# Optimization experiments

Hardware: AMD Instinct MI355X
Metric: run time of the kernel (lower is better)

Reference implementation:

```python
import jax, jax.numpy as jnp
import numpy as np

B, H, S, D = 4, 16, 2048, 64

def setup_inputs() -> dict:
    key = jax.random.key(0)
    kq, kk, kv = jax.random.split(key, 3)
    return {
        "query": jax.random.normal(kq, (B, H, S, D), dtype=jnp.float32),
        "key": jax.random.normal(kk, (B, H, S, D), dtype=jnp.float32),
        "value": jax.random.normal(kv, (B, H, S, D), dtype=jnp.float32),
        "dropout_p": 0,
    }

def reference(query, key, value, dropout_p):
    # qk: [B,H,S,S] materialized as in the original (unfused SDPA)
    scale = query.shape[-1] ** -0.5
    qk = jnp.einsum("bhqd,bhkd->bhqk", query, key) * scale
    attn = jax.nn.softmax(qk, axis=-1)
    # dropout_p == 0 -> identity (keeps reference deterministic)
    out = jnp.einsum("bhqk,bhkd->bhqd", attn, value)
    return out
```

## Files before the change

kernel.cpp:

```cpp
#include <hip/hip_runtime.h>
#include <hip/hip_bf16.h>

#define B_   4
#define H_   16
#define SEQ  2048
#define DH   64
#define BM   128
#define BN   128
#define NBH  (B_ * H_)
#define NELEM (NBH * SEQ * DH)

typedef __bf16 bf16x8 __attribute__((ext_vector_type(8)));
typedef float  f32x4  __attribute__((ext_vector_type(4)));
typedef unsigned short u16x8 __attribute__((ext_vector_type(8)));
typedef unsigned short u16x4 __attribute__((ext_vector_type(4)));

__device__ __forceinline__ unsigned short f2bu(float x) {
    __hip_bfloat16 h = __float2bfloat16(x);
    return __builtin_bit_cast(unsigned short, h);
}

__device__ __forceinline__ void ld_lds16(const unsigned short* g, unsigned short* l) {
    __builtin_amdgcn_global_load_lds(
        (const __attribute__((address_space(1))) unsigned int*)(g),
        (__attribute__((address_space(3))) unsigned int*)(l), 16, 0, 0);
}

__global__ __launch_bounds__(256)
void cvt_k_kernel(const float* __restrict__ K, unsigned short* __restrict__ Kb) {
    const int i = (blockIdx.x * 256 + threadIdx.x) * 8;
    const float4 a = *reinterpret_cast<const float4*>(K + i);
    const float4 b = *reinterpret_cast<const float4*>(K + i + 4);
    u16x8 o;
    o[0] = f2bu(a.x); o[1] = f2bu(a.y); o[2] = f2bu(a.z); o[3] = f2bu(a.w);
    o[4] = f2bu(b.x); o[5] = f2bu(b.y); o[6] = f2bu(b.z); o[7] = f2bu(b.w);
    *reinterpret_cast<u16x8*>(Kb + i) = o;
}

__global__ __launch_bounds__(256)
void tr_v_kernel(const float* __restrict__ V, unsigned short* __restrict__ Vt) {
    __shared__ unsigned short tile[64 * 72];
    const int bh = blockIdx.y;
    const int s0 = blockIdx.x * 64;
    const float* Vb = V + (size_t)bh * SEQ * DH + (size_t)s0 * DH;
    unsigned short* Vo = Vt + (size_t)bh * DH * SEQ;
    const int t = threadIdx.x;
    {
        const int sl = t >> 2, d0 = (t & 3) * 16;
        for (int c = 0; c < 4; ++c) {
            const float4 v = *reinterpret_cast<const float4*>(Vb + sl * DH + d0 + c * 4);
            u16x4 u; u[0] = f2bu(v.x); u[1] = f2bu(v.y); u[2] = f2bu(v.z); u[3] = f2bu(v.w);
            *reinterpret_cast<u16x4*>(&tile[sl * 72 + d0 + c * 4]) = u;
        }
    }
    __syncthreads();
    {
        const int d = t >> 2, sc = (t & 3) * 16;
        for (int j = 0; j < 4; ++j) {
            u16x4 u;
            u[0] = tile[(sc + 4 * j + 0) * 72 + d];
            u[1] = tile[(sc + 4 * j + 1) * 72 + d];
            u[2] = tile[(sc + 4 * j + 2) * 72 + d];
            u[3] = tile[(sc + 4 * j + 3) * 72 + d];
            *reinterpret_cast<u16x4*>(Vo + (size_t)d * SEQ + s0 + sc + 4 * j) = u;
        }
    }
}

__global__ __launch_bounds__(256, 2)
void fa_fwd(const float* __restrict__ Qg, const unsigned short* __restrict__ Kb,
            const unsigned short* __restrict__ Vtb, float* __restrict__ Og)
{
    __shared__ __attribute__((aligned(16))) unsigned short smem[32768];
    unsigned short* Klds = smem;
    unsigned short* Vlds = smem + 8192;
    unsigned short* Plds = smem + 16384;

    const int tid  = threadIdx.x;
    const int lane = tid & 63;
    const int wave = tid >> 6;
    const int l15  = lane & 15;
    const int quad = lane >> 4;

    const int qtile = blockIdx.x;
    const int bh    = blockIdx.y;

    const float*          Qb  = Qg  + (size_t)bh * SEQ * DH;
    const unsigned short* Kbh = Kb  + (size_t)bh * SEQ * DH;
    const unsigned short* Vbh = Vtb + (size_t)bh * DH * SEQ;
    float*                Ob  = Og  + (size_t)bh * SEQ * DH;

    const int qrow0 = qtile * BM + wave * 32;

    bf16x8 Qf[2][2];
    for (int rt = 0; rt < 2; ++rt) {
        const float* qsrc = Qb + (size_t)(qrow0 + rt * 16 + l15) * DH + quad * 8;
        for (int kt = 0; kt < 2; ++kt) {
            const float4 a = *reinterpret_cast<const float4*>(qsrc + kt * 32);
            const float4 b = *reinterpret_cast<const float4*>(qsrc + kt * 32 + 4);
            union { bf16x8 v; unsigned short u[8]; } tmp;
            tmp.u[0] = f2bu(a.x); tmp.u[1] = f2bu(a.y); tmp.u[2] = f2bu(a.z); tmp.u[3] = f2bu(a.w);
            tmp.u[4] = f2bu(b.x); tmp.u[5] = f2bu(b.y); tmp.u[6] = f2bu(b.z); tmp.u[7] = f2bu(b.w);
            Qf[rt][kt] = tmp.v;
        }
    }

    f32x4 Oacc[2][4];
    float lsum[2][4];
    for (int rt = 0; rt < 2; ++rt)
        for (int r = 0; r < 4; ++r) lsum[rt][r] = 0.f;
    for (int rt = 0; rt < 2; ++rt)
        for (int dt = 0; dt < 4; ++dt) {
            f32x4 z = {0.f, 0.f, 0.f, 0.f};
            Oacc[rt][dt] = z;
        }

    const float CS   = 0.125f * 1.4426950408889634f;
    const float MFIX = 12.0f;

    for (int it = 0; it < SEQ / BN; ++it) {
        __syncthreads();

        for (int i = 0; i < 4; ++i) {
            const int slot = i * 256 + tid;
            const int s = slot >> 3;
            const int g = (slot & 7) ^ (s & 7);
            ld_lds16(Kbh + (size_t)(it * BN + s) * DH + g * 8,
                     Klds + (size_t)(i * 256 + wave * 64) * 8);
        }
        for (int i = 0; i < 4; ++i) {
            const int slot = i * 256 + tid;
            const int d = slot >> 4;
            const int g = (slot & 15) ^ (d & 15);
            ld_lds16(Vbh + (size_t)d * SEQ + it * BN + g * 8,
                     Vlds + (size_t)(i * 256 + wave * 64) * 8);
        }
        __syncthreads();

        f32x4 Sacc[2][8];
        for (int rt = 0; rt < 2; ++rt)
            for (int nt = 0; nt < 8; ++nt) {
                f32x4 z = {0.f, 0.f, 0.f, 0.f};
                Sacc[rt][nt] = z;
            }
        for (int nt = 0; nt < 8; ++nt) {
            const int s  = nt * 16 + l15;
            const int sx = s & 7;
            const bf16x8 kf0 = *reinterpret_cast<const bf16x8*>(&Klds[s * 64 + ((quad    ) ^ sx) * 8]);
            const bf16x8 kf1 = *reinterpret_cast<const bf16x8*>(&Klds[s * 64 + ((quad + 4) ^ sx) * 8]);
            for (int rt = 0; rt < 2; ++rt) {
                Sacc[rt][nt] = __builtin_amdgcn_mfma_f32_16x16x32_bf16(Qf[rt][0], kf0, Sacc[rt][nt], 0, 0, 0);
                Sacc[rt][nt] = __builtin_amdgcn_mfma_f32_16x16x32_bf16(Qf[rt][1], kf1, Sacc[rt][nt], 0, 0, 0);
            }
        }

        for (int rt = 0; rt < 2; ++rt) {
            for (int r = 0; r < 4; ++r) {
                const int m  = wave * 32 + rt * 16 + quad * 4 + r;
                const int mx = m & 15;
                unsigned short* pb = &Plds[m << 7];
                float lacc = 0.f;
                for (int nt = 0; nt < 8; ++nt) {
                    const float p = __builtin_amdgcn_exp2f(fmaf(Sacc[rt][nt][r], CS, -MFIX));
                    lacc += p;
                    const int gg = nt * 2 + (l15 >> 3);
                    pb[((gg ^ mx) << 3) + (l15 & 7)] = f2bu(p);
                }
                lsum[rt][r] += lacc;
            }
        }

        for (int ks = 0; ks < 4; ++ks) {
            bf16x8 af[2];
            for (int rt = 0; rt < 2; ++rt) {
                const int m = wave * 32 + rt * 16 + l15;
                af[rt] = *reinterpret_cast<const bf16x8*>(
                    &Plds[(m << 7) + (((ks * 4 + quad) ^ l15) << 3)]);
            }
            for (int dt = 0; dt < 4; ++dt) {
                const int d = dt * 16 + l15;
                const bf16x8 bfr = *reinterpret_cast<const bf16x8*>(
                    &Vlds[(d << 7) + (((ks * 4 + quad) ^ l15) << 3)]);
                for (int rt = 0; rt < 2; ++rt)
                    Oacc[rt][dt] = __builtin_amdgcn_mfma_f32_16x16x32_bf16(af[rt], bfr, Oacc[rt][dt], 0, 0, 0);
            }
        }
    }

    for (int rt = 0; rt < 2; ++rt) {
        for (int r = 0; r < 4; ++r) {
            float tot = lsum[rt][r];
            tot += __shfl_xor(tot, 1, 64);
            tot += __shfl_xor(tot, 2, 64);
            tot += __shfl_xor(tot, 4, 64);
            tot += __shfl_xor(tot, 8, 64);
            const float inv = 1.0f / tot;
            const int row = qrow0 + rt * 16 + quad * 4 + r;
            float* orow = Ob + (size_t)row * DH + l15;
            for (int dt = 0; dt < 4; ++dt)
                orow[dt * 16] = Oacc[rt][dt][r] * inv;
        }
    }
}

extern "C" void kernel_launch(void* const* d_in, const int* in_sizes, int n_in,
                              void* d_out, int out_size, void* d_ws, size_t ws_size,
                              hipStream_t stream) {
    const float* Q = (const float*)d_in[0];
    const float* K = (const float*)d_in[1];
    const float* V = (const float*)d_in[2];
    float* O = (float*)d_out;

    unsigned short* Kb = (unsigned short*)d_ws;
    unsigned short* Vt = Kb + (size_t)NELEM;

    cvt_k_kernel<<<NELEM / (256 * 8), 256, 0, stream>>>(K, Kb);
    tr_v_kernel<<<dim3(SEQ / 64, NBH), 256, 0, stream>>>(V, Vt);
    fa_fwd<<<dim3(SEQ / BM, NBH), dim3(256), 0, stream>>>(Q, Kb, Vt, O);
}
```

Before: 245.5 us.

## Shrink P LDS buffer per wave, vectorize P stores, fuse K/V prep kernels

The K tile rows are loaded in a permuted order so each lane's eight softmax probabilities become contiguous keys and can be written to LDS as a single 16-byte store. The PV product is moved inside the per-row-tile loop, which halves the P staging buffer so total LDS drops and launch bounds can target three blocks per CU. The K conversion and V transpose preprocessing are fused into one launch. The trade-off is that the V fragments are now reloaded once per row tile, and register pressure rises at the higher occupancy target.

```diff
diff --git a/kernel.cpp b/kernel.cpp
--- a/kernel.cpp
+++ b/kernel.cpp
@@ -27,24 +27,26 @@
 }
 
 __global__ __launch_bounds__(256)
-void cvt_k_kernel(const float* __restrict__ K, unsigned short* __restrict__ Kb) {
-    const int i = (blockIdx.x * 256 + threadIdx.x) * 8;
-    const float4 a = *reinterpret_cast<const float4*>(K + i);
-    const float4 b = *reinterpret_cast<const float4*>(K + i + 4);
-    u16x8 o;
-    o[0] = f2bu(a.x); o[1] = f2bu(a.y); o[2] = f2bu(a.z); o[3] = f2bu(a.w);
-    o[4] = f2bu(b.x); o[5] = f2bu(b.y); o[6] = f2bu(b.z); o[7] = f2bu(b.w);
-    *reinterpret_cast<u16x8*>(Kb + i) = o;
-}
-
-__global__ __launch_bounds__(256)
-void tr_v_kernel(const float* __restrict__ V, unsigned short* __restrict__ Vt) {
+void prep_kv(const float* __restrict__ K, const float* __restrict__ V,
+             unsigned short* __restrict__ Kb, unsigned short* __restrict__ Vt) {
     __shared__ unsigned short tile[64 * 72];
     const int bh = blockIdx.y;
     const int s0 = blockIdx.x * 64;
+    const int t  = threadIdx.x;
+
+    {
+        const float* Ki = K + (size_t)bh * SEQ * DH + (size_t)s0 * DH;
+        unsigned short* Ko = Kb + (size_t)bh * SEQ * DH + (size_t)s0 * DH;
+        for (int j = 0; j < 4; ++j) {
+            const int e = (j * 256 + t) * 4;
+            const float4 v = *reinterpret_cast<const float4*>(Ki + e);
+            u16x4 u; u[0] = f2bu(v.x); u[1] = f2bu(v.y); u[2] = f2bu(v.z); u[3] = f2bu(v.w);
+            *reinterpret_cast<u16x4*>(Ko + e) = u;
+        }
+    }
+
     const float* Vb = V + (size_t)bh * SEQ * DH + (size_t)s0 * DH;
     unsigned short* Vo = Vt + (size_t)bh * DH * SEQ;
-    const int t = threadIdx.x;
     {
         const int sl = t >> 2, d0 = (t & 3) * 16;
         for (int c = 0; c < 4; ++c) {
@@ -67,11 +69,11 @@
     }
 }
 
-__global__ __launch_bounds__(256, 2)
+__global__ __launch_bounds__(256, 3)
 void fa_fwd(const float* __restrict__ Qg, const unsigned short* __restrict__ Kb,
             const unsigned short* __restrict__ Vtb, float* __restrict__ Og)
 {
-    __shared__ __attribute__((aligned(16))) unsigned short smem[32768];
+    __shared__ __attribute__((aligned(16))) unsigned short smem[24576];
     unsigned short* Klds = smem;
     unsigned short* Vlds = smem + 8192;
     unsigned short* Plds = smem + 16384;
@@ -122,16 +124,18 @@
         __syncthreads();
 
         for (int i = 0; i < 4; ++i) {
-            const int slot = i * 256 + tid;
-            const int s = slot >> 3;
-            const int g = (slot & 7) ^ (s & 7);
-            ld_lds16(Kbh + (size_t)(it * BN + s) * DH + g * 8,
+            const int beta = i * 256 + tid;
+            const int s    = beta >> 3;
+            const int b    = beta & 7;
+            const int gnat = b ^ (s & 7);
+            const int grow = (s & 15) * 8 + (s >> 4);
+            ld_lds16(Kbh + (size_t)(it * BN + grow) * DH + gnat * 8,
                      Klds + (size_t)(i * 256 + wave * 64) * 8);
         }
         for (int i = 0; i < 4; ++i) {
-            const int slot = i * 256 + tid;
-            const int d = slot >> 4;
-            const int g = (slot & 15) ^ (d & 15);
+            const int beta = i * 256 + tid;
+            const int d    = beta >> 4;
+            const int g    = (beta & 15) ^ (d & 15);
             ld_lds16(Vbh + (size_t)d * SEQ + it * BN + g * 8,
                      Vlds + (size_t)(i * 256 + wave * 64) * 8);
         }
@@ -156,33 +160,27 @@
 
         for (int rt = 0; rt < 2; ++rt) {
             for (int r = 0; r < 4; ++r) {
-                const int m  = wave * 32 + rt * 16 + quad * 4 + r;
-                const int mx = m & 15;
-                unsigned short* pb = &Plds[m << 7];
+                const int rho = quad * 4 + r;
+                unsigned short* pw = &Plds[((wave * 16 + rho) << 7) + ((l15 ^ rho) << 3)];
+                union { bf16x8 v; unsigned short u[8]; } prow;
                 float lacc = 0.f;
                 for (int nt = 0; nt < 8; ++nt) {
                     const float p = __builtin_amdgcn_exp2f(fmaf(Sacc[rt][nt][r], CS, -MFIX));
                     lacc += p;
-                    const int gg = nt * 2 + (l15 >> 3);
-                    pb[((gg ^ mx) << 3) + (l15 & 7)] = f2bu(p);
+                    prow.u[nt] = f2bu(p);
                 }
                 lsum[rt][r] += lacc;
-            }
-        }
-
-        for (int ks = 0; ks < 4; ++ks) {
-            bf16x8 af[2];
-            for (int rt = 0; rt < 2; ++rt) {
-                const int m = wave * 32 + rt * 16 + l15;
-                af[rt] = *reinterpret_cast<const bf16x8*>(
-                    &Plds[(m << 7) + (((ks * 4 + quad) ^ l15) << 3)]);
-            }
-            for (int dt = 0; dt < 4; ++dt) {
-                const int d = dt * 16 + l15;
-                const bf16x8 bfr = *reinterpret_cast<const bf16x8*>(
-                    &Vlds[(d << 7) + (((ks * 4 + quad) ^ l15) << 3)]);
-                for (int rt = 0; rt < 2; ++rt)
-                    Oacc[rt][dt] = __builtin_amdgcn_mfma_f32_16x16x32_bf16(af[rt], bfr, Oacc[rt][dt], 0, 0, 0);
+                *reinterpret_cast<bf16x8*>(pw) = prow.v;
+            }
+            for (int ks = 0; ks < 4; ++ks) {
+                const bf16x8 af = *reinterpret_cast<const bf16x8*>(
+                    &Plds[((wave * 16 + l15) << 7) + (((ks * 4 + quad) ^ l15) << 3)]);
+                for (int dt = 0; dt < 4; ++dt) {
+                    const int d = dt * 16 + l15;
+                    const bf16x8 bfr = *reinterpret_cast<const bf16x8*>(
+                        &Vlds[(d << 7) + (((ks * 4 + quad) ^ l15) << 3)]);
+                    Oacc[rt][dt] = __builtin_amdgcn_mfma_f32_16x16x32_bf16(af, bfr, Oacc[rt][dt], 0, 0, 0);
+                }
             }
         }
     }
@@ -214,7 +212,6 @@
     unsigned short* Kb = (unsigned short*)d_ws;
     unsigned short* Vt = Kb + (size_t)NELEM;
 
-    cvt_k_kernel<<<NELEM / (256 * 8), 256, 0, stream>>>(K, Kb);
-    tr_v_kernel<<<dim3(SEQ / 64, NBH), 256, 0, stream>>>(V, Vt);
+    prep_kv<<<dim3(SEQ / 64, NBH), 256, 0, stream>>>(K, V, Kb, Vt);
     fa_fwd<<<dim3(SEQ / BM, NBH), dim3(256), 0, stream>>>(Q, Kb, Vt, O);
 }
```

Measured after the change: 231.4 us. -5.7%, faster.
